# Performance work log

Measured on AMD Instinct MI355X. Metric: run time of the kernel, lower is better.

The kernel has to match this reference:

```python
import jax, jax.numpy as jnp
import numpy as np
from jax import lax

EPS = 1e-3  # Keras BatchNormalization default epsilon
DN = ('NHWC', 'HWIO', 'NHWC')


def _bn(x, gamma, beta, mean, var):
    inv = gamma * lax.rsqrt(var + EPS)
    return x * inv + (beta - mean * inv)


def setup_inputs() -> dict:
    key = jax.random.key(0)
    ks = jax.random.split(key, 5)
    B, H, W, C = 32, 56, 56, 256
    G, CG = 32, 4  # cardinality, channels per group
    CM = G * CG    # 128 mid channels
    x = jax.random.normal(ks[0], (B, H, W, C), jnp.float32)
    # 32 branch 1x1 convs (256->4 each) stacked -> one 256->128 conv
    w1 = jax.random.normal(ks[1], (1, 1, C, CM), jnp.float32) * 0.05
    b1 = jnp.zeros((CM,), jnp.float32)
    g1 = jnp.ones((CM,), jnp.float32)
    be1 = jnp.zeros((CM,), jnp.float32)
    m1 = jnp.zeros((CM,), jnp.float32)
    v1 = jnp.ones((CM,), jnp.float32)
    # 32 branch 3x3 convs (4->4 each) stacked -> grouped conv kernel [3,3,4,128]
    w2 = jax.random.normal(ks[2], (3, 3, CG, CM), jnp.float32) * 0.1
    b2 = jnp.zeros((CM,), jnp.float32)
    g2 = jnp.ones((CM,), jnp.float32)
    be2 = jnp.zeros((CM,), jnp.float32)
    m2 = jnp.zeros((CM,), jnp.float32)
    v2 = jnp.ones((CM,), jnp.float32)
    # final 1x1 conv 128 -> 256
    w3 = jax.random.normal(ks[3], (1, 1, CM, C), jnp.float32) * 0.05
    b3 = jnp.zeros((C,), jnp.float32)
    return dict(x=x, w1=w1, b1=b1, g1=g1, be1=be1, m1=m1, v1=v1,
                w2=w2, b2=b2, g2=g2, be2=be2, m2=m2, v2=v2,
                w3=w3, b3=b3)


def reference(x, w1, b1, g1, be1, m1, v1, w2, b2, g2, be2, m2, v2, w3, b3):
    # branch 1x1 convs fused: conv 256 -> 128
    h = lax.conv_general_dilated(x, w1, (1, 1), 'SAME', dimension_numbers=DN) + b1
    h = jax.nn.relu(_bn(h, g1, be1, m1, v1))
    # branch 3x3 convs fused: grouped conv, 32 groups of 4 channels
    h = lax.conv_general_dilated(h, w2, (1, 1), 'SAME', dimension_numbers=DN,
                                 feature_group_count=32) + b2
    h = jax.nn.relu(_bn(h, g2, be2, m2, v2))
    # Dropout(0.2) is identity at inference
    # final 1x1 conv 128 -> 256, residual add, relu
    out = lax.conv_general_dilated(h, w3, (1, 1), 'SAME', dimension_numbers=DN) + b3
    return jax.nn.relu(out + x)
```

## Files before the change

kernel.cpp:

```cpp
#include <hip/hip_runtime.h>
#include <stdint.h>

typedef unsigned short u16;
typedef unsigned int   u32;
typedef __attribute__((ext_vector_type(8))) short bf16x8;
typedef __attribute__((ext_vector_type(4))) float f32x4;

#define EPS 1e-3f
#define NB 32
#define HW 56
#define CI 256
#define CM 128
#define PIX (NB*HW*HW)

__device__ __forceinline__ float asf(u32 i){ union{u32 u; float f;} t; t.u=i; return t.f; }
__device__ __forceinline__ u16 f2bf(float f){
  union{float f; u32 u;} t; t.f = f;
  u32 x = t.u;
  return (u16)((x + 0x7fffu + ((x>>16)&1u)) >> 16);
}

__global__ __launch_bounds__(256) void kprep(
    const float* __restrict__ w1, const float* __restrict__ b1, const float* __restrict__ g1,
    const float* __restrict__ be1, const float* __restrict__ m1, const float* __restrict__ v1,
    const float* __restrict__ b2, const float* __restrict__ g2,
    const float* __restrict__ be2, const float* __restrict__ m2, const float* __restrict__ v2,
    const float* __restrict__ w3,
    u16* __restrict__ w1s, u16* __restrict__ w3s,
    float* __restrict__ A1, float* __restrict__ B1,
    float* __restrict__ A2, float* __restrict__ B2){
  int i = blockIdx.x*256 + threadIdx.x;
  if (i < 32768){
    {
      int j = i & 7, lane = (i >> 3) & 63, kt = (i >> 9) & 7, t = i >> 12;
      int col = lane & 15, quad = lane >> 4;
      int n = t*16 + col, k = kt*32 + quad*8 + j;
      w1s[i] = f2bf(w1[k*CM + n]);
    }
    {
      int j = i & 7, lane = (i >> 3) & 63, kc = (i >> 9) & 3, t = i >> 11;
      int col = lane & 15, quad = lane >> 4;
      int n = t*16 + col, k = kc*32 + quad*8 + j;
      w3s[i] = f2bf(w3[k*CI + n]);
    }
  }
  if (i < 128){
    float s1 = g1[i] * rsqrtf(v1[i] + EPS);
    A1[i] = s1;
    B1[i] = b1[i]*s1 + be1[i] - m1[i]*s1;
    float s2 = g2[i] * rsqrtf(v2[i] + EPS);
    A2[i] = s2;
    B2[i] = b2[i]*s2 + be2[i] - m2[i]*s2;
  }
}

#define K1_LS 72
__global__ __launch_bounds__(256) void k1(const float* __restrict__ x,
    const u16* __restrict__ w1s, const float* __restrict__ A1v,
    const float* __restrict__ B1v, u16* __restrict__ h1){
  __shared__ __align__(16) char smem[128*136*2];
  u16* As = (u16*)smem;
  const int tid  = threadIdx.x;
  const int lane = tid & 63, wv = tid >> 6;
  const int col  = lane & 15, quad = lane >> 4;
  const long p0 = (long)blockIdx.x * 128;
  f32x4 acc[8][2];
  #pragma unroll
  for (int a = 0; a < 8; a++)
    #pragma unroll
    for (int b = 0; b < 2; b++){ acc[a][b][0]=0.f; acc[a][b][1]=0.f; acc[a][b][2]=0.f; acc[a][b][3]=0.f; }
  for (int kc = 0; kc < 4; kc++){
    #pragma unroll
    for (int r = 0; r < 8; r++){
      int idx = r*256 + tid;
      int m = idx >> 4, f4 = idx & 15;
      float4 v = *(const float4*)(x + (p0+m)*CI + kc*64 + f4*4);
      u32 lo = (u32)f2bf(v.x) | ((u32)f2bf(v.y) << 16);
      u32 hi = (u32)f2bf(v.z) | ((u32)f2bf(v.w) << 16);
      *(uint2*)(As + m*K1_LS + f4*4) = make_uint2(lo, hi);
    }
    __syncthreads();
    #pragma unroll
    for (int ks = 0; ks < 2; ks++){
      const int kt = kc*2 + ks;
      bf16x8 bfr[2], af[8];
      #pragma unroll
      for (int nt = 0; nt < 2; nt++)
        bfr[nt] = *(const bf16x8*)(w1s + (size_t)(((wv*2+nt)*8 + kt)*64 + lane)*8);
      #pragma unroll
      for (int mt = 0; mt < 8; mt++)
        af[mt] = *(const bf16x8*)(As + (mt*16 + col)*K1_LS + ks*32 + quad*8);
      #pragma unroll
      for (int mt = 0; mt < 8; mt++)
        #pragma unroll
        for (int nt = 0; nt < 2; nt++)
          acc[mt][nt] = __builtin_amdgcn_mfma_f32_16x16x32_bf16(af[mt], bfr[nt], acc[mt][nt], 0, 0, 0);
    }
    __syncthreads();
  }
  u16* outw = (u16*)smem;
  #pragma unroll
  for (int nt = 0; nt < 2; nt++){
    int n = wv*32 + nt*16 + col;
    float a1 = A1v[n], b1v = B1v[n];
    #pragma unroll
    for (int mt = 0; mt < 8; mt++)
      #pragma unroll
      for (int reg = 0; reg < 4; reg++){
        int m = mt*16 + quad*4 + reg;
        outw[m*136 + n] = f2bf(fmaxf(acc[mt][nt][reg]*a1 + b1v, 0.f));
      }
  }
  __syncthreads();
  #pragma unroll
  for (int r = 0; r < 8; r++){
    int idx = r*256 + tid;
    int m = idx >> 4, u4 = idx & 15;
    uint4 v = *(const uint4*)(outw + m*136 + u4*8);
    *(uint4*)(h1 + (p0+m)*CM + u4*8) = v;
  }
}

#define LSH1 132
#define LSH2 136
__global__ __launch_bounds__(256) void k23(const u16* __restrict__ h1,
    const float* __restrict__ w2, const float* __restrict__ A2v,
    const float* __restrict__ B2v, const u16* __restrict__ w3s,
    const float* __restrict__ b3, const float* __restrict__ x,
    float* __restrict__ out){
  __shared__ __align__(16) char smem[3*HW*LSH1*2 + 64*LSH2*2 + 4608*4];
  u16*  tile = (u16*)smem;
  u16*  h2t  = (u16*)(smem + 3*HW*LSH1*2);
  float* wsh = (float*)(smem + 3*HW*LSH1*2 + 64*LSH2*2);
  float* pre = (float*)smem;

  const int tid = threadIdx.x;
  const int y0 = blockIdx.x % HW;
  const long p0 = (long)blockIdx.x * HW;

  for (int i = tid; i < 1152; i += 256)
    ((float4*)wsh)[i] = ((const float4*)w2)[i];
  for (int i = tid; i < 544; i += 256)
    ((u32*)(h2t + 56*LSH2))[i] = 0u;
  #pragma unroll
  for (int r = 0; r < 3; r++){
    const int yy = y0 + r - 1;
    const bool valid = (yy >= 0 && yy < HW);
    const uint4* src = (const uint4*)(h1 + (long)(blockIdx.x - y0 + yy)*HW*CM);
    for (int i = tid; i < 896; i += 256){
      uint4 v = make_uint4(0u,0u,0u,0u);
      if (valid) v = src[i];
      int px = i >> 4, ch = (i & 15)*8;
      u16* d = tile + (r*HW + px)*LSH1 + ch;
      *(uint2*)d     = make_uint2(v.x, v.y);
      *(uint2*)(d+4) = make_uint2(v.z, v.w);
    }
  }
  __syncthreads();

  {
    const int q   = tid >> 6;
    const int pos = tid & 63;
    if (pos < HW){
      int ixo[3]; u32 mk[3];
      #pragma unroll
      for (int kx = 0; kx < 3; kx++){
        int c = pos + kx - 1;
        ixo[kx] = (c < 0 ? 0 : (c > 55 ? 55 : c)) * LSH1;
        mk[kx] = (c >= 0 && c < HW) ? 0xffffffffu : 0u;
      }
      float acc[8][4];
      #pragma unroll
      for (int gi = 0; gi < 8; gi++){
        const int cb = (q*8 + gi)*4;
        float a0=0.f, a1=0.f, a2=0.f, a3=0.f;
        #pragma unroll
        for (int ky = 0; ky < 3; ky++){
          const u16* trow = tile + ky*HW*LSH1 + cb;
          #pragma unroll
          for (int kx = 0; kx < 3; kx++){
            uint2 hv = *(const uint2*)(trow + ixo[kx]);
            u32 hx = hv.x & mk[kx], hy = hv.y & mk[kx];
            float i0 = asf(hx<<16), i1 = asf(hx&0xffff0000u);
            float i2 = asf(hy<<16), i3 = asf(hy&0xffff0000u);
            const float* wp = wsh + ((ky*3+kx)*4)*CM + cb;
            float4 w0 = *(const float4*)(wp);
            float4 w1 = *(const float4*)(wp+CM);
            float4 wq2 = *(const float4*)(wp+2*CM);
            float4 wq3 = *(const float4*)(wp+3*CM);
            a0 += i0*w0.x + i1*w1.x + i2*wq2.x + i3*wq3.x;
            a1 += i0*w0.y + i1*w1.y + i2*wq2.y + i3*wq3.y;
            a2 += i0*w0.z + i1*w1.z + i2*wq2.z + i3*wq3.z;
            a3 += i0*w0.w + i1*w1.w + i2*wq2.w + i3*wq3.w;
          }
        }
        acc[gi][0]=a0; acc[gi][1]=a1; acc[gi][2]=a2; acc[gi][3]=a3;
      }
      u16 ov[32];
      #pragma unroll
      for (int gi = 0; gi < 8; gi++)
        #pragma unroll
        for (int co = 0; co < 4; co++){
          int c = q*32 + gi*4 + co;
          ov[gi*4+co] = f2bf(fmaxf(acc[gi][co]*A2v[c] + B2v[c], 0.f));
        }
      u16* op = h2t + pos*LSH2 + q*32;
      #pragma unroll
      for (int v4 = 0; v4 < 4; v4++){
        uint4 pk;
        pk.x = (u32)ov[v4*8+0] | ((u32)ov[v4*8+1]<<16);
        pk.y = (u32)ov[v4*8+2] | ((u32)ov[v4*8+3]<<16);
        pk.z = (u32)ov[v4*8+4] | ((u32)ov[v4*8+5]<<16);
        pk.w = (u32)ov[v4*8+6] | ((u32)ov[v4*8+7]<<16);
        *(uint4*)(op + v4*8) = pk;
      }
    }
  }
  __syncthreads();

  const int lane = tid & 63, wv = tid >> 6;
  const int col  = lane & 15, quad = lane >> 4;
  f32x4 acc3[4][4];
  #pragma unroll
  for (int a = 0; a < 4; a++)
    #pragma unroll
    for (int b = 0; b < 4; b++){ acc3[a][b][0]=0.f; acc3[a][b][1]=0.f; acc3[a][b][2]=0.f; acc3[a][b][3]=0.f; }
  float bias[4];
  #pragma unroll
  for (int nt = 0; nt < 4; nt++) bias[nt] = b3[wv*64 + nt*16 + col];
  #pragma unroll
  for (int kc = 0; kc < 4; kc++){
    bf16x8 bfr[4], af[4];
    #pragma unroll
    for (int nt = 0; nt < 4; nt++)
      bfr[nt] = *(const bf16x8*)(w3s + (size_t)(((wv*4+nt)*4 + kc)*64 + lane)*8);
    #pragma unroll
    for (int mt = 0; mt < 4; mt++)
      af[mt] = *(const bf16x8*)(h2t + (mt*16 + col)*LSH2 + kc*32 + quad*8);
    #pragma unroll
    for (int mt = 0; mt < 4; mt++)
      #pragma unroll
      for (int nt = 0; nt < 4; nt++)
        acc3[mt][nt] = __builtin_amdgcn_mfma_f32_16x16x32_bf16(af[mt], bfr[nt], acc3[mt][nt], 0, 0, 0);
  }
  const int wh = wv >> 1;
  const int nb = (wv & 1) * 64;
  #pragma unroll
  for (int h = 0; h < 2; h++){
    if (wh == h){
      #pragma unroll
      for (int mt = 0; mt < 4; mt++)
        #pragma unroll
        for (int nt = 0; nt < 4; nt++)
          #pragma unroll
          for (int reg = 0; reg < 4; reg++){
            int m = mt*16 + quad*4 + reg;
            pre[m*132 + nb + nt*16 + col] = acc3[mt][nt][reg] + bias[nt];
          }
    }
    __syncthreads();
    for (int i = tid; i < 1792; i += 256){
      int m = i >> 5, f4 = i & 31;
      float4 pv = *(const float4*)(pre + m*132 + f4*4);
      float4 xv = *(const float4*)(x + (p0+m)*CI + h*128 + f4*4);
      float4 o;
      o.x = fmaxf(pv.x + xv.x, 0.f);
      o.y = fmaxf(pv.y + xv.y, 0.f);
      o.z = fmaxf(pv.z + xv.z, 0.f);
      o.w = fmaxf(pv.w + xv.w, 0.f);
      *(float4*)(out + (p0+m)*CI + h*128 + f4*4) = o;
    }
    __syncthreads();
  }
}

extern "C" void kernel_launch(void* const* d_in, const int* in_sizes, int n_in,
                              void* d_out, int out_size, void* d_ws, size_t ws_size,
                              hipStream_t stream){
  (void)in_sizes; (void)n_in; (void)out_size; (void)ws_size;
  const float* x   = (const float*)d_in[0];
  const float* w1  = (const float*)d_in[1];
  const float* b1  = (const float*)d_in[2];
  const float* g1  = (const float*)d_in[3];
  const float* be1 = (const float*)d_in[4];
  const float* m1  = (const float*)d_in[5];
  const float* v1  = (const float*)d_in[6];
  const float* w2  = (const float*)d_in[7];
  const float* b2  = (const float*)d_in[8];
  const float* g2  = (const float*)d_in[9];
  const float* be2 = (const float*)d_in[10];
  const float* m2  = (const float*)d_in[11];
  const float* v2  = (const float*)d_in[12];
  const float* w3  = (const float*)d_in[13];
  const float* b3  = (const float*)d_in[14];

  char* ws = (char*)d_ws;
  u16* h1  = (u16*)ws;
  u16* w1s = (u16*)(ws + (size_t)PIX*CM*2);
  u16* w3s = w1s + 32768;
  float* A1 = (float*)(w3s + 32768);
  float* B1 = A1 + 128;
  float* A2 = B1 + 128;
  float* B2 = A2 + 128;

  kprep<<<128, 256, 0, stream>>>(w1,b1,g1,be1,m1,v1,b2,g2,be2,m2,v2,w3,
                                 w1s,w3s,A1,B1,A2,B2);
  k1<<<PIX/128, 256, 0, stream>>>(x, w1s, A1, B1, h1);
  k23<<<NB*HW, 256, 0, stream>>>(h1, w2, A2, B2, w3s, b3, x, (float*)d_out);
}
```

Before: 281.5 us.

## Load x directly into MFMA fragments in k1, widen k23 to 512 threads

k1 now has each wave load its A operands straight from global x into registers and convert them to bf16, dropping the LDS staging and the per-chunk barriers. Each wave now owns 32 rows and all 128 output columns. k23 runs with 512 threads and a blockIdx swizzle. It reuses the input tile's LDS for h2 to cut shared memory, and prefetches the residual x into registers before the grouped conv so global latency overlaps compute. The risks are more redundant global reads of x in k1 across waves and higher register pressure under the new launch bounds.

```diff
diff --git a/kernel.cpp b/kernel.cpp
--- a/kernel.cpp
+++ b/kernel.cpp
@@ -54,60 +54,49 @@
   }
 }
 
-#define K1_LS 72
-__global__ __launch_bounds__(256) void k1(const float* __restrict__ x,
+__global__ __launch_bounds__(256, 3) void k1(const float* __restrict__ x,
     const u16* __restrict__ w1s, const float* __restrict__ A1v,
     const float* __restrict__ B1v, u16* __restrict__ h1){
-  __shared__ __align__(16) char smem[128*136*2];
-  u16* As = (u16*)smem;
+  __shared__ __align__(16) u16 outw[128*136];
   const int tid  = threadIdx.x;
   const int lane = tid & 63, wv = tid >> 6;
   const int col  = lane & 15, quad = lane >> 4;
   const long p0 = (long)blockIdx.x * 128;
-  f32x4 acc[8][2];
-  #pragma unroll
-  for (int a = 0; a < 8; a++)
-    #pragma unroll
-    for (int b = 0; b < 2; b++){ acc[a][b][0]=0.f; acc[a][b][1]=0.f; acc[a][b][2]=0.f; acc[a][b][3]=0.f; }
-  for (int kc = 0; kc < 4; kc++){
-    #pragma unroll
-    for (int r = 0; r < 8; r++){
-      int idx = r*256 + tid;
-      int m = idx >> 4, f4 = idx & 15;
-      float4 v = *(const float4*)(x + (p0+m)*CI + kc*64 + f4*4);
-      u32 lo = (u32)f2bf(v.x) | ((u32)f2bf(v.y) << 16);
-      u32 hi = (u32)f2bf(v.z) | ((u32)f2bf(v.w) << 16);
-      *(uint2*)(As + m*K1_LS + f4*4) = make_uint2(lo, hi);
-    }
-    __syncthreads();
-    #pragma unroll
-    for (int ks = 0; ks < 2; ks++){
-      const int kt = kc*2 + ks;
-      bf16x8 bfr[2], af[8];
-      #pragma unroll
-      for (int nt = 0; nt < 2; nt++)
-        bfr[nt] = *(const bf16x8*)(w1s + (size_t)(((wv*2+nt)*8 + kt)*64 + lane)*8);
-      #pragma unroll
-      for (int mt = 0; mt < 8; mt++)
-        af[mt] = *(const bf16x8*)(As + (mt*16 + col)*K1_LS + ks*32 + quad*8);
-      #pragma unroll
-      for (int mt = 0; mt < 8; mt++)
-        #pragma unroll
-        for (int nt = 0; nt < 2; nt++)
-          acc[mt][nt] = __builtin_amdgcn_mfma_f32_16x16x32_bf16(af[mt], bfr[nt], acc[mt][nt], 0, 0, 0);
-    }
-    __syncthreads();
-  }
-  u16* outw = (u16*)smem;
-  #pragma unroll
-  for (int nt = 0; nt < 2; nt++){
-    int n = wv*32 + nt*16 + col;
+  f32x4 acc[2][8];
+  #pragma unroll
+  for (int a = 0; a < 2; a++)
+    #pragma unroll
+    for (int b = 0; b < 8; b++){ acc[a][b][0]=0.f; acc[a][b][1]=0.f; acc[a][b][2]=0.f; acc[a][b][3]=0.f; }
+  const float* xb = x + (p0 + wv*32 + col)*CI + quad*8;
+  for (int kt = 0; kt < 8; kt++){
+    bf16x8 bfr[8];
+    #pragma unroll
+    for (int nt = 0; nt < 8; nt++)
+      bfr[nt] = *(const bf16x8*)(w1s + (size_t)((nt*8 + kt)*64 + lane)*8);
+    #pragma unroll
+    for (int mt = 0; mt < 2; mt++){
+      const float* xp = xb + mt*16*CI + kt*32;
+      float4 v0 = *(const float4*)xp;
+      float4 v1 = *(const float4*)(xp + 4);
+      union{ bf16x8 v; u32 w[4]; } af;
+      af.w[0] = (u32)f2bf(v0.x) | ((u32)f2bf(v0.y) << 16);
+      af.w[1] = (u32)f2bf(v0.z) | ((u32)f2bf(v0.w) << 16);
+      af.w[2] = (u32)f2bf(v1.x) | ((u32)f2bf(v1.y) << 16);
+      af.w[3] = (u32)f2bf(v1.z) | ((u32)f2bf(v1.w) << 16);
+      #pragma unroll
+      for (int nt = 0; nt < 8; nt++)
+        acc[mt][nt] = __builtin_amdgcn_mfma_f32_16x16x32_bf16(af.v, bfr[nt], acc[mt][nt], 0, 0, 0);
+    }
+  }
+  #pragma unroll
+  for (int nt = 0; nt < 8; nt++){
+    int n = nt*16 + col;
     float a1 = A1v[n], b1v = B1v[n];
     #pragma unroll
-    for (int mt = 0; mt < 8; mt++)
+    for (int mt = 0; mt < 2; mt++)
       #pragma unroll
       for (int reg = 0; reg < 4; reg++){
-        int m = mt*16 + quad*4 + reg;
+        int m = wv*32 + mt*16 + quad*4 + reg;
         outw[m*136 + n] = f2bf(fmaxf(acc[mt][nt][reg]*a1 + b1v, 0.f));
       }
   }
@@ -123,31 +112,31 @@
 
 #define LSH1 132
 #define LSH2 136
-__global__ __launch_bounds__(256) void k23(const u16* __restrict__ h1,
+__global__ __launch_bounds__(512, 4) void k23(const u16* __restrict__ h1,
     const float* __restrict__ w2, const float* __restrict__ A2v,
     const float* __restrict__ B2v, const u16* __restrict__ w3s,
     const float* __restrict__ b3, const float* __restrict__ x,
     float* __restrict__ out){
-  __shared__ __align__(16) char smem[3*HW*LSH1*2 + 64*LSH2*2 + 4608*4];
+  __shared__ __align__(16) char smem[3*HW*LSH1*2 + 4608*4];
   u16*  tile = (u16*)smem;
-  u16*  h2t  = (u16*)(smem + 3*HW*LSH1*2);
-  float* wsh = (float*)(smem + 3*HW*LSH1*2 + 64*LSH2*2);
+  u16*  h2t  = (u16*)smem;
   float* pre = (float*)smem;
+  float* wsh = (float*)(smem + 3*HW*LSH1*2);
 
   const int tid = threadIdx.x;
-  const int y0 = blockIdx.x % HW;
-  const long p0 = (long)blockIdx.x * HW;
-
-  for (int i = tid; i < 1152; i += 256)
+  const int bid = blockIdx.x;
+  const int blk = (bid & 7)*224 + (bid >> 3);
+  const int y0 = blk % HW;
+  const long p0 = (long)blk * HW;
+
+  for (int i = tid; i < 1152; i += 512)
     ((float4*)wsh)[i] = ((const float4*)w2)[i];
-  for (int i = tid; i < 544; i += 256)
-    ((u32*)(h2t + 56*LSH2))[i] = 0u;
   #pragma unroll
   for (int r = 0; r < 3; r++){
     const int yy = y0 + r - 1;
     const bool valid = (yy >= 0 && yy < HW);
-    const uint4* src = (const uint4*)(h1 + (long)(blockIdx.x - y0 + yy)*HW*CM);
-    for (int i = tid; i < 896; i += 256){
+    const uint4* src = (const uint4*)(h1 + (long)(blk - y0 + yy)*HW*CM);
+    for (int i = tid; i < 896; i += 512){
       uint4 v = make_uint4(0u,0u,0u,0u);
       if (valid) v = src[i];
       int px = i >> 4, ch = (i & 15)*8;
@@ -158,119 +147,169 @@
   }
   __syncthreads();
 
-  {
-    const int q   = tid >> 6;
-    const int pos = tid & 63;
-    if (pos < HW){
-      int ixo[3]; u32 mk[3];
-      #pragma unroll
-      for (int kx = 0; kx < 3; kx++){
-        int c = pos + kx - 1;
-        ixo[kx] = (c < 0 ? 0 : (c > 55 ? 55 : c)) * LSH1;
-        mk[kx] = (c >= 0 && c < HW) ? 0xffffffffu : 0u;
+  float4 xr[4];
+  #pragma unroll
+  for (int it = 0; it < 4; it++){
+    int i = tid + it*512;
+    if (i < 1792){
+      int m = i >> 5, f4 = i & 31;
+      xr[it] = *(const float4*)(x + (p0+m)*CI + f4*4);
+    }
+  }
+
+  const int q = tid >> 6, pos = tid & 63;
+  const bool act = pos < HW;
+  u16 ov[16];
+  if (act){
+    int ixo[3]; u32 mk[3];
+    #pragma unroll
+    for (int kx = 0; kx < 3; kx++){
+      int c = pos + kx - 1;
+      ixo[kx] = (c < 0 ? 0 : (c > 55 ? 55 : c)) * LSH1;
+      mk[kx] = (c >= 0 && c < HW) ? 0xffffffffu : 0u;
+    }
+    #pragma unroll
+    for (int gi = 0; gi < 4; gi++){
+      const int cb = q*16 + gi*4;
+      float a0=0.f, a1=0.f, a2=0.f, a3=0.f;
+      #pragma unroll
+      for (int ky = 0; ky < 3; ky++){
+        const u16* trow = tile + ky*HW*LSH1 + cb;
+        #pragma unroll
+        for (int kx = 0; kx < 3; kx++){
+          uint2 hv = *(const uint2*)(trow + ixo[kx]);
+          u32 hx = hv.x & mk[kx], hy = hv.y & mk[kx];
+          float i0 = asf(hx<<16), i1 = asf(hx&0xffff0000u);
+          float i2 = asf(hy<<16), i3 = asf(hy&0xffff0000u);
+          const float* wp = wsh + ((ky*3+kx)*4)*CM + cb;
+          float4 w0  = *(const float4*)(wp);
+          float4 w1v = *(const float4*)(wp+CM);
+          float4 w2v = *(const float4*)(wp+2*CM);
+          float4 w3v = *(const float4*)(wp+3*CM);
+          a0 += i0*w0.x + i1*w1v.x + i2*w2v.x + i3*w3v.x;
+          a1 += i0*w0.y + i1*w1v.y + i2*w2v.y + i3*w3v.y;
+          a2 += i0*w0.z + i1*w1v.z + i2*w2v.z + i3*w3v.z;
+          a3 += i0*w0.w + i1*w1v.w + i2*w2v.w + i3*w3v.w;
+        }
       }
-      float acc[8][4];
-      #pragma unroll
-      for (int gi = 0; gi < 8; gi++){
-        const int cb = (q*8 + gi)*4;
-        float a0=0.f, a1=0.f, a2=0.f, a3=0.f;
-        #pragma unroll
-        for (int ky = 0; ky < 3; ky++){
-          const u16* trow = tile + ky*HW*LSH1 + cb;
-          #pragma unroll
-          for (int kx = 0; kx < 3; kx++){
-            uint2 hv = *(const uint2*)(trow + ixo[kx]);
-            u32 hx = hv.x & mk[kx], hy = hv.y & mk[kx];
-            float i0 = asf(hx<<16), i1 = asf(hx&0xffff0000u);
-            float i2 = asf(hy<<16), i3 = asf(hy&0xffff0000u);
-            const float* wp = wsh + ((ky*3+kx)*4)*CM + cb;
-            float4 w0 = *(const float4*)(wp);
-            float4 w1 = *(const float4*)(wp+CM);
-            float4 wq2 = *(const float4*)(wp+2*CM);
-            float4 wq3 = *(const float4*)(wp+3*CM);
-            a0 += i0*w0.x + i1*w1.x + i2*wq2.x + i3*wq3.x;
-            a1 += i0*w0.y + i1*w1.y + i2*wq2.y + i3*wq3.y;
-            a2 += i0*w0.z + i1*w1.z + i2*wq2.z + i3*wq3.z;
-            a3 += i0*w0.w + i1*w1.w + i2*wq2.w + i3*wq3.w;
-          }
-        }
-        acc[gi][0]=a0; acc[gi][1]=a1; acc[gi][2]=a2; acc[gi][3]=a3;
+      float av[4] = {a0, a1, a2, a3};
+      #pragma unroll
+      for (int co = 0; co < 4; co++){
+        int c = cb + co;
+        ov[gi*4+co] = f2bf(fmaxf(av[co]*A2v[c] + B2v[c], 0.f));
       }
-      u16 ov[32];
-      #pragma unroll
-      for (int gi = 0; gi < 8; gi++)
-        #pragma unroll
-        for (int co = 0; co < 4; co++){
-          int c = q*32 + gi*4 + co;
-          ov[gi*4+co] = f2bf(fmaxf(acc[gi][co]*A2v[c] + B2v[c], 0.f));
-        }
-      u16* op = h2t + pos*LSH2 + q*32;
-      #pragma unroll
-      for (int v4 = 0; v4 < 4; v4++){
-        uint4 pk;
-        pk.x = (u32)ov[v4*8+0] | ((u32)ov[v4*8+1]<<16);
-        pk.y = (u32)ov[v4*8+2] | ((u32)ov[v4*8+3]<<16);
-        pk.z = (u32)ov[v4*8+4] | ((u32)ov[v4*8+5]<<16);
-        pk.w = (u32)ov[v4*8+6] | ((u32)ov[v4*8+7]<<16);
-        *(uint4*)(op + v4*8) = pk;
-      }
-    }
-  }
+    }
+  }
+  __syncthreads();
+
+  if (act){
+    uint4 pk0, pk1;
+    pk0.x = (u32)ov[0]  | ((u32)ov[1]<<16);
+    pk0.y = (u32)ov[2]  | ((u32)ov[3]<<16);
+    pk0.z = (u32)ov[4]  | ((u32)ov[5]<<16);
+    pk0.w = (u32)ov[6]  | ((u32)ov[7]<<16);
+    pk1.x = (u32)ov[8]  | ((u32)ov[9]<<16);
+    pk1.y = (u32)ov[10] | ((u32)ov[11]<<16);
+    pk1.z = (u32)ov[12] | ((u32)ov[13]<<16);
+    pk1.w = (u32)ov[14] | ((u32)ov[15]<<16);
+    u16* op = h2t + pos*LSH2 + q*16;
+    *(uint4*)op     = pk0;
+    *(uint4*)(op+8) = pk1;
+  }
+  for (int i = tid; i < 544; i += 512)
+    ((u32*)(h2t + 56*LSH2))[i] = 0u;
   __syncthreads();
 
   const int lane = tid & 63, wv = tid >> 6;
   const int col  = lane & 15, quad = lane >> 4;
-  f32x4 acc3[4][4];
+  f32x4 acc3[4][2];
   #pragma unroll
   for (int a = 0; a < 4; a++)
     #pragma unroll
-    for (int b = 0; b < 4; b++){ acc3[a][b][0]=0.f; acc3[a][b][1]=0.f; acc3[a][b][2]=0.f; acc3[a][b][3]=0.f; }
-  float bias[4];
-  #pragma unroll
-  for (int nt = 0; nt < 4; nt++) bias[nt] = b3[wv*64 + nt*16 + col];
+    for (int b = 0; b < 2; b++){ acc3[a][b][0]=0.f; acc3[a][b][1]=0.f; acc3[a][b][2]=0.f; acc3[a][b][3]=0.f; }
+  float bias[2];
+  #pragma unroll
+  for (int nt = 0; nt < 2; nt++) bias[nt] = b3[wv*32 + nt*16 + col];
   #pragma unroll
   for (int kc = 0; kc < 4; kc++){
-    bf16x8 bfr[4], af[4];
-    #pragma unroll
-    for (int nt = 0; nt < 4; nt++)
-      bfr[nt] = *(const bf16x8*)(w3s + (size_t)(((wv*4+nt)*4 + kc)*64 + lane)*8);
+    bf16x8 bfr[2], af[4];
+    #pragma unroll
+    for (int nt = 0; nt < 2; nt++)
+      bfr[nt] = *(const bf16x8*)(w3s + (size_t)(((wv*2+nt)*4 + kc)*64 + lane)*8);
     #pragma unroll
     for (int mt = 0; mt < 4; mt++)
       af[mt] = *(const bf16x8*)(h2t + (mt*16 + col)*LSH2 + kc*32 + quad*8);
     #pragma unroll
     for (int mt = 0; mt < 4; mt++)
       #pragma unroll
-      for (int nt = 0; nt < 4; nt++)
+      for (int nt = 0; nt < 2; nt++)
         acc3[mt][nt] = __builtin_amdgcn_mfma_f32_16x16x32_bf16(af[mt], bfr[nt], acc3[mt][nt], 0, 0, 0);
   }
-  const int wh = wv >> 1;
-  const int nb = (wv & 1) * 64;
-  #pragma unroll
-  for (int h = 0; h < 2; h++){
-    if (wh == h){
-      #pragma unroll
-      for (int mt = 0; mt < 4; mt++)
+  __syncthreads();
+
+  if (wv < 4){
+    #pragma unroll
+    for (int mt = 0; mt < 4; mt++)
+      #pragma unroll
+      for (int nt = 0; nt < 2; nt++)
         #pragma unroll
-        for (int nt = 0; nt < 4; nt++)
-          #pragma unroll
-          for (int reg = 0; reg < 4; reg++){
-            int m = mt*16 + quad*4 + reg;
-            pre[m*132 + nb + nt*16 + col] = acc3[mt][nt][reg] + bias[nt];
-          }
-    }
-    __syncthreads();
-    for (int i = tid; i < 1792; i += 256){
+        for (int reg = 0; reg < 4; reg++){
+          int m = mt*16 + quad*4 + reg;
+          pre[m*132 + (wv&3)*32 + nt*16 + col] = acc3[mt][nt][reg] + bias[nt];
+        }
+  }
+  __syncthreads();
+
+  float4 xr2[4];
+  #pragma unroll
+  for (int it = 0; it < 4; it++){
+    int i = tid + it*512;
+    if (i < 1792){
+      int m = i >> 5, f4 = i & 31;
+      xr2[it] = *(const float4*)(x + (p0+m)*CI + 128 + f4*4);
+    }
+  }
+  #pragma unroll
+  for (int it = 0; it < 4; it++){
+    int i = tid + it*512;
+    if (i < 1792){
       int m = i >> 5, f4 = i & 31;
       float4 pv = *(const float4*)(pre + m*132 + f4*4);
-      float4 xv = *(const float4*)(x + (p0+m)*CI + h*128 + f4*4);
       float4 o;
-      o.x = fmaxf(pv.x + xv.x, 0.f);
-      o.y = fmaxf(pv.y + xv.y, 0.f);
-      o.z = fmaxf(pv.z + xv.z, 0.f);
-      o.w = fmaxf(pv.w + xv.w, 0.f);
-      *(float4*)(out + (p0+m)*CI + h*128 + f4*4) = o;
-    }
-    __syncthreads();
+      o.x = fmaxf(pv.x + xr[it].x, 0.f);
+      o.y = fmaxf(pv.y + xr[it].y, 0.f);
+      o.z = fmaxf(pv.z + xr[it].z, 0.f);
+      o.w = fmaxf(pv.w + xr[it].w, 0.f);
+      *(float4*)(out + (p0+m)*CI + f4*4) = o;
+    }
+  }
+  __syncthreads();
+
+  if (wv >= 4){
+    #pragma unroll
+    for (int mt = 0; mt < 4; mt++)
+      #pragma unroll
+      for (int nt = 0; nt < 2; nt++)
+        #pragma unroll
+        for (int reg = 0; reg < 4; reg++){
+          int m = mt*16 + quad*4 + reg;
+          pre[m*132 + (wv&3)*32 + nt*16 + col] = acc3[mt][nt][reg] + bias[nt];
+        }
+  }
+  __syncthreads();
+  #pragma unroll
+  for (int it = 0; it < 4; it++){
+    int i = tid + it*512;
+    if (i < 1792){
+      int m = i >> 5, f4 = i & 31;
+      float4 pv = *(const float4*)(pre + m*132 + f4*4);
+      float4 o;
+      o.x = fmaxf(pv.x + xr2[it].x, 0.f);
+      o.y = fmaxf(pv.y + xr2[it].y, 0.f);
+      o.z = fmaxf(pv.z + xr2[it].z, 0.f);
+      o.w = fmaxf(pv.w + xr2[it].w, 0.f);
+      *(float4*)(out + (p0+m)*CI + 128 + f4*4) = o;
+    }
   }
 }
 
@@ -306,5 +345,5 @@
   kprep<<<128, 256, 0, stream>>>(w1,b1,g1,be1,m1,v1,b2,g2,be2,m2,v2,w3,
                                  w1s,w3s,A1,B1,A2,B2);
   k1<<<PIX/128, 256, 0, stream>>>(x, w1s, A1, B1, h1);
-  k23<<<NB*HW, 256, 0, stream>>>(h1, w2, A2, B2, w3s, b3, x, (float*)d_out);
-}
+  k23<<<NB*HW, 512, 0, stream>>>(h1, w2, A2, B2, w3s, b3, x, (float*)d_out);
+}
```

Measured after the change: 287.6 us. 2.2% more time.

## Process two output rows per k23 block with 512 threads and swizzled LDS

Applied to the files above, without the earlier changes.

Each k23 block now covers two image rows (112 pixels) using 512 threads, so it loads a 4-row halo instead of 3 rows per output row. That removes a third of the redundant h1 reads and amortises the w2 weight staging over twice the work. The intermediate h2 tile is reused in place of the input tile with an XOR swizzle to avoid LDS bank conflicts, and block indices are remapped to spread neighbouring rows. This needs an extra barrier and uses more registers and LDS per block, which may cut occupancy.

```diff
diff --git a/kernel.cpp b/kernel.cpp
--- a/kernel.cpp
+++ b/kernel.cpp
@@ -122,32 +122,31 @@
 }
 
 #define LSH1 132
-#define LSH2 136
-__global__ __launch_bounds__(256) void k23(const u16* __restrict__ h1,
+__global__ __launch_bounds__(512, 2) void k23(const u16* __restrict__ h1,
     const float* __restrict__ w2, const float* __restrict__ A2v,
     const float* __restrict__ B2v, const u16* __restrict__ w3s,
     const float* __restrict__ b3, const float* __restrict__ x,
     float* __restrict__ out){
-  __shared__ __align__(16) char smem[3*HW*LSH1*2 + 64*LSH2*2 + 4608*4];
+  __shared__ __align__(16) char smem[4*HW*LSH1*2 + 4608*4];
   u16*  tile = (u16*)smem;
-  u16*  h2t  = (u16*)(smem + 3*HW*LSH1*2);
-  float* wsh = (float*)(smem + 3*HW*LSH1*2 + 64*LSH2*2);
+  char* h2t  = smem;
   float* pre = (float*)smem;
+  float* wsh = (float*)(smem + 4*HW*LSH1*2);
 
   const int tid = threadIdx.x;
-  const int y0 = blockIdx.x % HW;
-  const long p0 = (long)blockIdx.x * HW;
-
-  for (int i = tid; i < 1152; i += 256)
+  const int bid = blockIdx.x;
+  const int blk = (bid & 7)*112 + (bid >> 3);
+  const int y0 = (blk % 28) * 2;
+  const long p0 = (long)blk * 112;
+
+  for (int i = tid; i < 1152; i += 512)
     ((float4*)wsh)[i] = ((const float4*)w2)[i];
-  for (int i = tid; i < 544; i += 256)
-    ((u32*)(h2t + 56*LSH2))[i] = 0u;
-  #pragma unroll
-  for (int r = 0; r < 3; r++){
+  #pragma unroll
+  for (int r = 0; r < 4; r++){
     const int yy = y0 + r - 1;
     const bool valid = (yy >= 0 && yy < HW);
-    const uint4* src = (const uint4*)(h1 + (long)(blockIdx.x - y0 + yy)*HW*CM);
-    for (int i = tid; i < 896; i += 256){
+    const uint4* src = (const uint4*)(h1 + ((long)p0 + (r-1)*HW)*CM);
+    for (int i = tid; i < 896; i += 512){
       uint4 v = make_uint4(0u,0u,0u,0u);
       if (valid) v = src[i];
       int px = i >> 4, ch = (i & 15)*8;
@@ -158,25 +157,26 @@
   }
   __syncthreads();
 
-  {
-    const int q   = tid >> 6;
-    const int pos = tid & 63;
-    if (pos < HW){
-      int ixo[3]; u32 mk[3];
-      #pragma unroll
-      for (int kx = 0; kx < 3; kx++){
-        int c = pos + kx - 1;
-        ixo[kx] = (c < 0 ? 0 : (c > 55 ? 55 : c)) * LSH1;
-        mk[kx] = (c >= 0 && c < HW) ? 0xffffffffu : 0u;
-      }
-      float acc[8][4];
-      #pragma unroll
-      for (int gi = 0; gi < 8; gi++){
-        const int cb = (q*8 + gi)*4;
+  const int q = tid >> 6, pos = tid & 63;
+  const bool act = pos < HW;
+  u16 ov[2][16];
+  if (act){
+    int ixo[3]; u32 mk[3];
+    #pragma unroll
+    for (int kx = 0; kx < 3; kx++){
+      int c = pos + kx - 1;
+      ixo[kx] = (c < 0 ? 0 : (c > 55 ? 55 : c)) * LSH1;
+      mk[kx] = (c >= 0 && c < HW) ? 0xffffffffu : 0u;
+    }
+    #pragma unroll
+    for (int rr = 0; rr < 2; rr++){
+      #pragma unroll
+      for (int gi = 0; gi < 4; gi++){
+        const int cb = q*16 + gi*4;
         float a0=0.f, a1=0.f, a2=0.f, a3=0.f;
         #pragma unroll
         for (int ky = 0; ky < 3; ky++){
-          const u16* trow = tile + ky*HW*LSH1 + cb;
+          const u16* trow = tile + (rr+ky)*HW*LSH1 + cb;
           #pragma unroll
           for (int kx = 0; kx < 3; kx++){
             uint2 hv = *(const uint2*)(trow + ixo[kx]);
@@ -184,35 +184,40 @@
             float i0 = asf(hx<<16), i1 = asf(hx&0xffff0000u);
             float i2 = asf(hy<<16), i3 = asf(hy&0xffff0000u);
             const float* wp = wsh + ((ky*3+kx)*4)*CM + cb;
-            float4 w0 = *(const float4*)(wp);
-            float4 w1 = *(const float4*)(wp+CM);
-            float4 wq2 = *(const float4*)(wp+2*CM);
-            float4 wq3 = *(const float4*)(wp+3*CM);
-            a0 += i0*w0.x + i1*w1.x + i2*wq2.x + i3*wq3.x;
-            a1 += i0*w0.y + i1*w1.y + i2*wq2.y + i3*wq3.y;
-            a2 += i0*w0.z + i1*w1.z + i2*wq2.z + i3*wq3.z;
-            a3 += i0*w0.w + i1*w1.w + i2*wq2.w + i3*wq3.w;
+            float4 w0  = *(const float4*)(wp);
+            float4 w1v = *(const float4*)(wp+CM);
+            float4 w2v = *(const float4*)(wp+2*CM);
+            float4 w3v = *(const float4*)(wp+3*CM);
+            a0 += i0*w0.x + i1*w1v.x + i2*w2v.x + i3*w3v.x;
+            a1 += i0*w0.y + i1*w1v.y + i2*w2v.y + i3*w3v.y;
+            a2 += i0*w0.z + i1*w1v.z + i2*w2v.z + i3*w3v.z;
+            a3 += i0*w0.w + i1*w1v.w + i2*w2v.w + i3*w3v.w;
           }
         }
-        acc[gi][0]=a0; acc[gi][1]=a1; acc[gi][2]=a2; acc[gi][3]=a3;
-      }
-      u16 ov[32];
-      #pragma unroll
-      for (int gi = 0; gi < 8; gi++)
+        float av[4] = {a0, a1, a2, a3};
         #pragma unroll
         for (int co = 0; co < 4; co++){
-          int c = q*32 + gi*4 + co;
-          ov[gi*4+co] = f2bf(fmaxf(acc[gi][co]*A2v[c] + B2v[c], 0.f));
+          int c = cb + co;
+          ov[rr][gi*4+co] = f2bf(fmaxf(av[co]*A2v[c] + B2v[c], 0.f));
         }
-      u16* op = h2t + pos*LSH2 + q*32;
-      #pragma unroll
-      for (int v4 = 0; v4 < 4; v4++){
+      }
+    }
+  }
+  __syncthreads();
+
+  if (act){
+    #pragma unroll
+    for (int rr = 0; rr < 2; rr++){
+      int m = rr*HW + pos;
+      #pragma unroll
+      for (int hh = 0; hh < 2; hh++){
         uint4 pk;
-        pk.x = (u32)ov[v4*8+0] | ((u32)ov[v4*8+1]<<16);
-        pk.y = (u32)ov[v4*8+2] | ((u32)ov[v4*8+3]<<16);
-        pk.z = (u32)ov[v4*8+4] | ((u32)ov[v4*8+5]<<16);
-        pk.w = (u32)ov[v4*8+6] | ((u32)ov[v4*8+7]<<16);
-        *(uint4*)(op + v4*8) = pk;
+        pk.x = (u32)ov[rr][hh*8+0] | ((u32)ov[rr][hh*8+1]<<16);
+        pk.y = (u32)ov[rr][hh*8+2] | ((u32)ov[rr][hh*8+3]<<16);
+        pk.z = (u32)ov[rr][hh*8+4] | ((u32)ov[rr][hh*8+5]<<16);
+        pk.w = (u32)ov[rr][hh*8+6] | ((u32)ov[rr][hh*8+7]<<16);
+        int byte = m*256 + ((q*32 + hh*16) ^ ((m & 7) << 4));
+        *(uint4*)(h2t + byte) = pk;
       }
     }
   }
@@ -220,49 +225,51 @@
 
   const int lane = tid & 63, wv = tid >> 6;
   const int col  = lane & 15, quad = lane >> 4;
-  f32x4 acc3[4][4];
-  #pragma unroll
-  for (int a = 0; a < 4; a++)
-    #pragma unroll
-    for (int b = 0; b < 4; b++){ acc3[a][b][0]=0.f; acc3[a][b][1]=0.f; acc3[a][b][2]=0.f; acc3[a][b][3]=0.f; }
-  float bias[4];
-  #pragma unroll
-  for (int nt = 0; nt < 4; nt++) bias[nt] = b3[wv*64 + nt*16 + col];
+  f32x4 acc3[7][2];
+  #pragma unroll
+  for (int a = 0; a < 7; a++)
+    #pragma unroll
+    for (int b = 0; b < 2; b++){ acc3[a][b][0]=0.f; acc3[a][b][1]=0.f; acc3[a][b][2]=0.f; acc3[a][b][3]=0.f; }
+  float bias[2];
+  #pragma unroll
+  for (int nt = 0; nt < 2; nt++) bias[nt] = b3[wv*32 + nt*16 + col];
   #pragma unroll
   for (int kc = 0; kc < 4; kc++){
-    bf16x8 bfr[4], af[4];
-    #pragma unroll
-    for (int nt = 0; nt < 4; nt++)
-      bfr[nt] = *(const bf16x8*)(w3s + (size_t)(((wv*4+nt)*4 + kc)*64 + lane)*8);
-    #pragma unroll
-    for (int mt = 0; mt < 4; mt++)
-      af[mt] = *(const bf16x8*)(h2t + (mt*16 + col)*LSH2 + kc*32 + quad*8);
-    #pragma unroll
-    for (int mt = 0; mt < 4; mt++)
-      #pragma unroll
-      for (int nt = 0; nt < 4; nt++)
-        acc3[mt][nt] = __builtin_amdgcn_mfma_f32_16x16x32_bf16(af[mt], bfr[nt], acc3[mt][nt], 0, 0, 0);
-  }
-  const int wh = wv >> 1;
-  const int nb = (wv & 1) * 64;
+    bf16x8 bfr[2];
+    #pragma unroll
+    for (int nt = 0; nt < 2; nt++)
+      bfr[nt] = *(const bf16x8*)(w3s + (size_t)(((wv*2+nt)*4 + kc)*64 + lane)*8);
+    #pragma unroll
+    for (int mt = 0; mt < 7; mt++){
+      int row = mt*16 + col;
+      bf16x8 af = *(const bf16x8*)(h2t + row*256 + ((kc*64 + quad*16) ^ ((row & 7) << 4)));
+      #pragma unroll
+      for (int nt = 0; nt < 2; nt++)
+        acc3[mt][nt] = __builtin_amdgcn_mfma_f32_16x16x32_bf16(af, bfr[nt], acc3[mt][nt], 0, 0, 0);
+    }
+  }
+  __syncthreads();
+
   #pragma unroll
   for (int h = 0; h < 2; h++){
-    if (wh == h){
-      #pragma unroll
-      for (int mt = 0; mt < 4; mt++)
+    if ((wv >> 2) == h){
+      #pragma unroll
+      for (int mt = 0; mt < 7; mt++)
         #pragma unroll
-        for (int nt = 0; nt < 4; nt++)
+        for (int nt = 0; nt < 2; nt++)
           #pragma unroll
           for (int reg = 0; reg < 4; reg++){
             int m = mt*16 + quad*4 + reg;
-            pre[m*132 + nb + nt*16 + col] = acc3[mt][nt][reg] + bias[nt];
+            pre[m*132 + (wv&3)*32 + nt*16 + col] = acc3[mt][nt][reg] + bias[nt];
           }
     }
     __syncthreads();
-    for (int i = tid; i < 1792; i += 256){
+    #pragma unroll
+    for (int it = 0; it < 7; it++){
+      int i = tid + it*512;
       int m = i >> 5, f4 = i & 31;
+      float4 xv = *(const float4*)(x + (p0+m)*CI + h*128 + f4*4);
       float4 pv = *(const float4*)(pre + m*132 + f4*4);
-      float4 xv = *(const float4*)(x + (p0+m)*CI + h*128 + f4*4);
       float4 o;
       o.x = fmaxf(pv.x + xv.x, 0.f);
       o.y = fmaxf(pv.y + xv.y, 0.f);
@@ -306,5 +313,5 @@
   kprep<<<128, 256, 0, stream>>>(w1,b1,g1,be1,m1,v1,b2,g2,be2,m2,v2,w3,
                                  w1s,w3s,A1,B1,A2,B2);
   k1<<<PIX/128, 256, 0, stream>>>(x, w1s, A1, B1, h1);
-  k23<<<NB*HW, 256, 0, stream>>>(h1, w2, A2, B2, w3s, b3, x, (float*)d_out);
-}
+  k23<<<NB*28, 512, 0, stream>>>(h1, w2, A2, B2, w3s, b3, x, (float*)d_out);
+}
```

After: 510.3 us. 81.3% more time.
